# Kernel tuning notes

Hardware: AMD Instinct MI355X
Metric: run time of the kernel (lower is better)

Reference implementation:

```python
import jax, jax.numpy as jnp
import numpy as np

CONV1_T = 15.0
CONV2_T = 10.0
K2, R2 = 8, 1

def conv2d(x, w):
    # x: [T,C,H,W] (time as batch), w: [O,I,kh,kw], VALID conv (SpykeTorch Convolution = F.conv2d)
    return jax.lax.conv_general_dilated(x, w, (1, 1), 'VALID',
                                        dimension_numbers=('NCHW', 'OIHW', 'NCHW'))

def pad2(x, p):
    return jnp.pad(x, ((0, 0), (0, 0), (p, p), (p, p)))

def maxpool(x, k, s):
    return jax.lax.reduce_window(x, -jnp.inf, jax.lax.max,
                                 (1, 1, k, k), (1, 1, s, s), 'VALID')

def fire(pot, thr):
    # torch.threshold_(pot, thr, 0): keep value iff value > thr
    tp = jnp.where(pot > thr, pot, 0.0)
    return jnp.sign(tp), tp

def pointwise_inhibition(pot):
    # pot: [T,C,H,W] thresholded potentials (>=0). At each spatial position, only the
    # channel that spikes earliest (ties broken by max potential) survives.
    T, C, H, W = pot.shape
    maxval = jnp.max(pot, axis=1, keepdims=True)                    # [T,1,H,W]
    argmax = jnp.argmax(pot, axis=1, keepdims=True)                 # [T,1,H,W]
    clamp = jnp.sign(maxval)                                        # spike indicator per t
    first_t = jnp.clip((T - clamp.sum(axis=0, keepdims=True)).astype(jnp.int32), 0, T - 1)  # [1,1,H,W]
    winners = jnp.take_along_axis(argmax, first_t, axis=0)          # [1,1,H,W] winning channel
    spiked = clamp[-1:]                                             # [1,1,H,W] any spike at all
    ch = jnp.arange(C).reshape(1, C, 1, 1)
    coef = jnp.where(ch == winners, spiked, 0.0)                    # [1,C,H,W] one-hot * spiked
    return pot * coef

def get_k_winners(pot, spikes, kwta, radius):
    # Iterative k-winner selection with per-winner feature suppression and
    # columnar (spatial) inhibition of radius `radius`. Returns [kwta,3] (c,h,w), -1 if invalid.
    T, C, H, W = pot.shape
    first_t = jnp.clip((T - spikes.sum(axis=0, keepdims=True)).astype(jnp.int32), 0, T - 1)
    values = jnp.take_along_axis(pot, first_t, axis=0)              # earliest potential per (c,h,w)
    trunc = spikes * values
    v = jnp.max(trunc) * T
    trunc = trunc + spikes * v                                      # earlier spikes -> larger sum
    total = trunc.sum(axis=0)                                       # [C,H,W]

    rows = jnp.arange(H)[None, :, None]
    cols = jnp.arange(W)[None, None, :]
    chs = jnp.arange(C)[:, None, None]

    def step(total, _):
        flat = total.reshape(-1)
        idx = jnp.argmax(flat)
        max_val = flat[idx]
        c = idx // (H * W)
        h = (idx % (H * W)) // W
        w = idx % W
        valid = max_val != 0
        mask = (chs == c)
        if radius > 0:
            mask = mask | ((jnp.abs(rows - h) <= radius) & (jnp.abs(cols - w) <= radius))
        new_total = jnp.where(valid & mask, 0.0, total)
        winner = jnp.where(valid,
                           jnp.stack([c, h, w]).astype(jnp.int32),
                           jnp.full((3,), -1, jnp.int32))
        return new_total, winner

    _, winners = jax.lax.scan(step, total, None, length=kwta)
    return winners  # [kwta,3]

def setup_inputs() -> dict:
    key = jax.random.key(0)
    ka, kb, kc = jax.random.split(key, 3)
    T, C, H, W = 15, 6, 256, 256
    # cumulative (spike-wise accumulated) binary spike trains, SpykeTorch convention
    events = (jax.random.uniform(ka, (T, C, H, W)) < 0.02).astype(jnp.float32)
    x = jnp.sign(jnp.cumsum(events, axis=0))
    w1 = 0.8 + 0.05 * jax.random.normal(kb, (30, 6, 5, 5), dtype=jnp.float32)
    w2 = 0.8 + 0.05 * jax.random.normal(kc, (250, 30, 3, 3), dtype=jnp.float32)
    return {"x": x, "w1": w1, "w2": w2, "max_layer": 2}

def reference(x, w1, w2, max_layer):
    # training path, max_layer == 2 (static)
    x = pad2(x, 2)
    pot = conv2d(x, w1)                                  # [15,30,256,256]
    spk, pot = fire(pot, CONV1_T)
    spk_in = pad2(maxpool(spk, 2, 2), 1)                 # [15,30,130,130]
    pot = conv2d(spk_in, w2)                             # [15,250,128,128]
    spk, pot = fire(pot, CONV2_T)
    pot = pointwise_inhibition(pot)
    spk = jnp.sign(pot)
    winners = get_k_winners(pot, spk, K2, R2)
    return spk, pot, winners
```

## Files before the change

kernel.cpp:

```cpp
#include <hip/hip_runtime.h>
#include <cstdint>
#include <cstddef>

#define HW 16384
typedef float v2f __attribute__((ext_vector_type(2)));
typedef __attribute__((ext_vector_type(4))) float f32x4_t;
typedef __attribute__((ext_vector_type(8))) short bf16x8;

__device__ __forceinline__ unsigned short f2bf(float f) {
  unsigned int u = __float_as_uint(f);
  unsigned int r = (u + 0x7FFFu + ((u >> 16) & 1u)) >> 16;
  return (unsigned short)r;
}

__global__ __launch_bounds__(256) void k_packw(const float* __restrict__ w1,
                                               const float* __restrict__ w2,
                                               v2f* __restrict__ w1p,
                                               unsigned short* __restrict__ Wpk) {
  int g = blockIdx.x * 256 + threadIdx.x;
  if (g < 9216) {
    int mt = g / 576;
    int rem = g - mt * 576;
    int kc = rem >> 6, lane = rem & 63;
    int oc = mt * 16 + (lane & 15);
    unsigned int hbits[4], mbits[4], lbits[4];
#pragma unroll
    for (int p = 0; p < 4; ++p) { hbits[p] = 0; mbits[p] = 0; lbits[p] = 0; }
#pragma unroll
    for (int jj = 0; jj < 8; ++jj) {
      int k = kc * 32 + ((lane >> 4) << 3) + jj;
      float val = (oc < 250 && k < 270) ? w2[(size_t)oc * 270 + k] : 0.f;
      unsigned short h = f2bf(val);
      float r1 = val - __uint_as_float((unsigned int)h << 16);
      unsigned short m = f2bf(r1);
      float r2 = r1 - __uint_as_float((unsigned int)m << 16);
      unsigned short l = f2bf(r2);
      hbits[jj >> 1] |= (unsigned int)h << ((jj & 1) * 16);
      mbits[jj >> 1] |= (unsigned int)m << ((jj & 1) * 16);
      lbits[jj >> 1] |= (unsigned int)l << ((jj & 1) * 16);
    }
    size_t off = (size_t)g * 24;
    *(uint4*)&Wpk[off] = make_uint4(hbits[0], hbits[1], hbits[2], hbits[3]);
    *(uint4*)&Wpk[off + 8] = make_uint4(mbits[0], mbits[1], mbits[2], mbits[3]);
    *(uint4*)&Wpk[off + 16] = make_uint4(lbits[0], lbits[1], lbits[2], lbits[3]);
    return;
  }
  int i = g - 9216;
  if (i < 2250) {
    int m = i % 3, k = (i / 3) % 25, ic = (i / 75) % 6, ocg = i / 450;
    int g0 = ocg * 6 + 2 * m;
    w1p[i] = (v2f){w1[(g0 * 6 + ic) * 25 + k], w1[((g0 + 1) * 6 + ic) * 25 + k]};
  }
}

__global__ __launch_bounds__(256, 4) void k_conv1(const float* __restrict__ x,
                                                  const v2f* __restrict__ w1p,
                                                  uint8_t* __restrict__ spk_pool) {
  const int tile = blockIdx.x, ocg = blockIdx.y, t = blockIdx.z;
  const int oc0 = ocg * 6;
  const int tid = threadIdx.x;
  const int tx = tid & 15, ty = tid >> 4;
  const int px0 = (tile & 7) << 4, py0 = (tile >> 3) << 4;
  __shared__ float sx[2][36 * 38];
  const int iy0 = (py0 << 1) - 2, ix0 = (px0 << 1) - 2;

  int goff[6], soff[6];
  bool act[6];
#pragma unroll
  for (int j = 0; j < 6; ++j) {
    int idx = tid + 256 * j;
    bool a = idx < 1296;
    int r = idx / 36, c = idx - r * 36;
    int gy = iy0 + r, gx = ix0 + c;
    bool inb = a && (unsigned)gy < 256u && (unsigned)gx < 256u;
    goff[j] = inb ? ((gy << 8) + gx) : -1;
    soff[j] = a ? (r * 38 + c) : 0;
    act[j] = a;
  }

  v2f acc2[3][4];
#pragma unroll
  for (int m = 0; m < 3; ++m)
#pragma unroll
    for (int j = 0; j < 4; ++j) acc2[m][j] = (v2f){0.f, 0.f};

  const float* xt = x + ((size_t)(t * 6) << 16);
  float v[6];
#pragma unroll
  for (int j = 0; j < 6; ++j) v[j] = (goff[j] >= 0) ? xt[goff[j]] : 0.f;
#pragma unroll
  for (int j = 0; j < 6; ++j)
    if (act[j]) sx[0][soff[j]] = v[j];
  __syncthreads();

  for (int ic = 0; ic < 6; ++ic) {
    const int cur = ic & 1, nxt = cur ^ 1;
    if (ic < 5) {
      const float* xp = xt + ((size_t)(ic + 1) << 16);
#pragma unroll
      for (int j = 0; j < 6; ++j) v[j] = (goff[j] >= 0) ? xp[goff[j]] : 0.f;
    }
    float win_[6][6];
#pragma unroll
    for (int r = 0; r < 6; ++r) {
      float2 a = *(const float2*)&sx[cur][(2 * ty + r) * 38 + 2 * tx];
      float2 b = *(const float2*)&sx[cur][(2 * ty + r) * 38 + 2 * tx + 2];
      float2 c = *(const float2*)&sx[cur][(2 * ty + r) * 38 + 2 * tx + 4];
      win_[r][0] = a.x; win_[r][1] = a.y; win_[r][2] = b.x;
      win_[r][3] = b.y; win_[r][4] = c.x; win_[r][5] = c.y;
    }
    const v2f* wp = w1p + ((size_t)(ocg * 6 + ic) * 25) * 3;
#pragma unroll
    for (int k = 0; k < 25; ++k) {
      const int ky = k / 5, kx = k % 5;
      v2f s0 = (v2f){win_[ky][kx], win_[ky][kx]};
      v2f s1 = (v2f){win_[ky][kx + 1], win_[ky][kx + 1]};
      v2f s2 = (v2f){win_[ky + 1][kx], win_[ky + 1][kx]};
      v2f s3 = (v2f){win_[ky + 1][kx + 1], win_[ky + 1][kx + 1]};
#pragma unroll
      for (int m = 0; m < 3; ++m) {
        v2f wv = wp[k * 3 + m];
        acc2[m][0] += wv * s0;
        acc2[m][1] += wv * s1;
        acc2[m][2] += wv * s2;
        acc2[m][3] += wv * s3;
      }
    }
    if (ic < 5) {
#pragma unroll
      for (int j = 0; j < 6; ++j)
        if (act[j]) sx[nxt][soff[j]] = v[j];
    }
    __syncthreads();
  }
#pragma unroll
  for (int g = 0; g < 6; ++g) {
    const int m = g >> 1;
    float a0 = (g & 1) ? acc2[m][0].y : acc2[m][0].x;
    float a1 = (g & 1) ? acc2[m][1].y : acc2[m][1].x;
    float a2 = (g & 1) ? acc2[m][2].y : acc2[m][2].x;
    float a3 = (g & 1) ? acc2[m][3].y : acc2[m][3].x;
    int spike = (a0 > 15.f) || (a1 > 15.f) || (a2 > 15.f) || (a3 > 15.f);
    spk_pool[((size_t)(t * 30 + oc0 + g) << 14) + ((size_t)(py0 + ty) << 7) + (px0 + tx)] =
        (uint8_t)spike;
  }
}

__global__ __launch_bounds__(256, 3) void k_conv2(const uint8_t* __restrict__ spk_pool,
                                                  const unsigned short* __restrict__ Wpk,
                                                  float* __restrict__ pot2,
                                                  unsigned long long* __restrict__ mp) {
  const int nt = blockIdx.x, t = blockIdx.y;
  const int y = nt >> 1, x0 = (nt & 1) << 6;
  const int tid = threadIdx.x;
  __shared__ unsigned short Bs[64 * 288];
  __shared__ unsigned char raw[30 * 3 * 68];
  __shared__ unsigned long long mx[64];
  if (tid < 64) mx[tid] = 0ULL;

  for (int idx = tid; idx < 30 * 204; idx += 256) {
    int ic = idx / 204;
    int rem = idx - ic * 204;
    int row = rem / 68, col = rem - row * 68;
    int gy = y - 1 + row, gx = x0 - 1 + col;
    unsigned char v = 0;
    if ((unsigned)gy < 128u && (unsigned)gx < 128u && col < 67)
      v = spk_pool[((size_t)(t * 30 + ic) << 14) + (gy << 7) + gx];
    raw[idx] = v;
  }
  __syncthreads();

  {
    const int n = tid & 63, q = tid >> 6;
#pragma unroll
    for (int c = 0; c < 9; ++c) {
      unsigned int bits[4] = {0u, 0u, 0u, 0u};
#pragma unroll
      for (int e = 0; e < 8; ++e) {
        const int m = c * 8 + e;
        const int mc = m / 9, tap = m - mc * 9;
        const int dy = tap / 3, dx = tap - dy * 3;
        const int ic = q * 8 + mc;
        unsigned int v = 0u;
        if (ic < 30)
          v = raw[ic * 204 + dy * 68 + n + dx] ? 0x3F80u : 0u;
        bits[e >> 1] |= v << ((e & 1) * 16);
      }
      *(uint4*)&Bs[n * 288 + q * 72 + c * 8] = make_uint4(bits[0], bits[1], bits[2], bits[3]);
    }
  }
  __syncthreads();

  const int w = tid >> 6, lane = tid & 63;
  const int bcol = lane & 15, bq = lane >> 4;
  f32x4_t acc[4][4];
#pragma unroll
  for (int i = 0; i < 4; ++i)
#pragma unroll
    for (int j = 0; j < 4; ++j) acc[i][j] = (f32x4_t){0.f, 0.f, 0.f, 0.f};

  for (int kc = 0; kc < 9; ++kc) {
    bf16x8 bb[4];
#pragma unroll
    for (int j = 0; j < 4; ++j)
      bb[j] = *(const bf16x8*)&Bs[(j * 16 + bcol) * 288 + kc * 32 + bq * 8];
    bf16x8 ah[4], am[4], al[4];
#pragma unroll
    for (int i = 0; i < 4; ++i) {
      const size_t off = (size_t)(((w * 4 + i) * 9 + kc) * 64 + lane) * 24;
      ah[i] = *(const bf16x8*)&Wpk[off];
      am[i] = *(const bf16x8*)&Wpk[off + 8];
      al[i] = *(const bf16x8*)&Wpk[off + 16];
    }
#pragma unroll
    for (int i = 0; i < 4; ++i)
#pragma unroll
      for (int j = 0; j < 4; ++j) {
        acc[i][j] = __builtin_amdgcn_mfma_f32_16x16x32_bf16(ah[i], bb[j], acc[i][j], 0, 0, 0);
        acc[i][j] = __builtin_amdgcn_mfma_f32_16x16x32_bf16(am[i], bb[j], acc[i][j], 0, 0, 0);
        acc[i][j] = __builtin_amdgcn_mfma_f32_16x16x32_bf16(al[i], bb[j], acc[i][j], 0, 0, 0);
      }
  }

#pragma unroll
  for (int j = 0; j < 4; ++j) {
    const int loc = (y << 7) + x0 + j * 16 + bcol;
    unsigned long long best = 0ULL;
#pragma unroll
    for (int i = 0; i < 4; ++i) {
      const int mt = w * 4 + i;
#pragma unroll
      for (int r = 0; r < 4; ++r) {
        const int oc = mt * 16 + (bq << 2) + r;
        float v = acc[i][j][r];
        v = v > 10.f ? v : 0.f;
        if (oc < 250) {
          pot2[((size_t)(t * 250 + oc) << 14) + loc] = v;
          unsigned long long pk =
              ((unsigned long long)__float_as_uint(v) << 32) |
              (unsigned long long)(1023 - oc);
          best = pk > best ? pk : best;
        }
      }
    }
    atomicMax(&mx[j * 16 + bcol], best);
  }
  __syncthreads();
  if (tid < 64) mp[(size_t)t * HW + (y << 7) + x0 + tid] = mx[tid];
}

__global__ __launch_bounds__(64) void k_inhib(const float* __restrict__ pot2,
                                              const unsigned long long* __restrict__ mp,
                                              int* __restrict__ win,
                                              float* __restrict__ nspv,
                                              float* __restrict__ valv,
                                              float* __restrict__ sv) {
  const int loc = (blockIdx.x << 6) + threadIdx.x;
  int cnt = 0;
  float last = 0.f;
  unsigned long long pks[15];
#pragma unroll
  for (int t = 0; t < 15; ++t) {
    pks[t] = mp[t * HW + loc];
    float v = __uint_as_float((unsigned)(pks[t] >> 32));
    cnt += (v > 0.f) ? 1 : 0;
    if (t == 14) last = v;
  }
  const int spiked = (last > 0.f) ? 1 : 0;
  int ft = 15 - cnt;
  if (ft > 14) ft = 14;
  if (ft < 0) ft = 0;
  int wc = 1023 - (int)(pks[ft] & 1023ULL);
  if ((unsigned)wc > 249u) wc = 0;
  int nsp = 0;
#pragma unroll
  for (int t = 0; t < 15; ++t) {
    float v = pot2[((size_t)(t * 250 + wc) << 14) + loc];
    v = spiked ? v : 0.f;
    sv[t * HW + loc] = v;
    nsp += (v > 0.f) ? 1 : 0;
  }
  int ft2 = 15 - nsp;
  if (ft2 > 14) ft2 = 14;
  float value = spiked ? pot2[((size_t)(ft2 * 250 + wc) << 14) + loc] : 0.f;
  win[loc] = spiked ? wc : -1;
  nspv[loc] = (float)nsp;
  valv[loc] = value;
}

__global__ __launch_bounds__(256) void k_final(const int* __restrict__ win,
                                               const float* __restrict__ sv,
                                               float* __restrict__ spk_out,
                                               float* __restrict__ pot_out) {
  const int t = blockIdx.y;
  const int loc = (blockIdx.x << 8) + threadIdx.x;
  const int wcL = win[loc];
  const float v = sv[t * HW + loc];
  const float s = (v > 0.f) ? 1.f : 0.f;
  float* pp = pot_out + ((size_t)(t * 250) << 14) + loc;
  float* sp = spk_out + ((size_t)(t * 250) << 14) + loc;
  for (int c = 0; c < 250; ++c) {
    pp[(size_t)c << 14] = (c == wcL) ? v : 0.f;
    sp[(size_t)c << 14] = (c == wcL) ? s : 0.f;
  }
}

__global__ __launch_bounds__(256) void k_select(const int* __restrict__ win,
                                                const float* __restrict__ nspv,
                                                const float* __restrict__ valv,
                                                float* __restrict__ winners) {
  __shared__ float tot[HW];
  __shared__ int wchan[HW];
  __shared__ float redV[256];
  __shared__ int redK[256];
  __shared__ float bcValid[1];
  __shared__ int bcKey[1];
  const int tid = threadIdx.x;

  float lmax = 0.f;
  for (int i = tid; i < HW; i += 256) {
    wchan[i] = win[i];
    lmax = fmaxf(lmax, valv[i]);
  }
  redV[tid] = lmax;
  __syncthreads();
  for (int s = 128; s > 0; s >>= 1) {
    if (tid < s) redV[tid] = fmaxf(redV[tid], redV[tid + s]);
    __syncthreads();
  }
  const float v15 = redV[0] * 15.f;
  __syncthreads();
  for (int i = tid; i < HW; i += 256) tot[i] = nspv[i] * (valv[i] + v15);
  __syncthreads();

  for (int k = 0; k < 8; ++k) {
    float bv = -1.f;
    int bkey = 0x7fffffff;
    for (int i = tid; i < HW; i += 256) {
      float v = tot[i];
      int key = (wchan[i] << 14) + i;
      if (v > bv || (v == bv && key < bkey)) { bv = v; bkey = key; }
    }
    redV[tid] = bv;
    redK[tid] = bkey;
    __syncthreads();
    for (int s = 128; s > 0; s >>= 1) {
      if (tid < s) {
        float ov = redV[tid + s];
        int ok = redK[tid + s];
        if (ov > redV[tid] || (ov == redV[tid] && ok < redK[tid])) {
          redV[tid] = ov;
          redK[tid] = ok;
        }
      }
      __syncthreads();
    }
    if (tid == 0) {
      float mv = redV[0];
      int mk = redK[0];
      int valid = (mv != 0.f) ? 1 : 0;
      int c = mk >> 14, l = mk & (HW - 1);
      winners[k * 3 + 0] = valid ? (float)c : -1.f;
      winners[k * 3 + 1] = valid ? (float)(l >> 7) : -1.f;
      winners[k * 3 + 2] = valid ? (float)(l & 127) : -1.f;
      bcValid[0] = valid ? 1.f : 0.f;
      bcKey[0] = mk;
    }
    __syncthreads();
    if (bcValid[0] > 0.f) {
      int mk = bcKey[0];
      int c = mk >> 14, h = (mk & (HW - 1)) >> 7, w = mk & 127;
      for (int i = tid; i < HW; i += 256) {
        int hh = i >> 7, ww = i & 127;
        int dh = hh - h; if (dh < 0) dh = -dh;
        int dw = ww - w; if (dw < 0) dw = -dw;
        bool m = (wchan[i] == c) || (dh <= 1 && dw <= 1);
        if (m) tot[i] = 0.f;
      }
    }
    __syncthreads();
  }
}

extern "C" void kernel_launch(void* const* d_in, const int* in_sizes, int n_in,
                              void* d_out, int out_size, void* d_ws, size_t ws_size,
                              hipStream_t stream) {
  const float* x = (const float*)d_in[0];
  const float* w1 = (const float*)d_in[1];
  const float* w2 = (const float*)d_in[2];
  (void)in_sizes; (void)n_in; (void)out_size; (void)ws_size;

  float* spk_out = (float*)d_out;
  float* pot_out = spk_out + 61440000;
  float* winners = spk_out + 122880000;

  uint8_t* ws = (uint8_t*)d_ws;
  unsigned long long* mp = (unsigned long long*)ws;
  uint8_t* spk_pool = ws + 1966080;
  int* win = (int*)(ws + 9338880);
  float* nspv = (float*)(ws + 9404416);
  float* valv = (float*)(ws + 9469952);
  float* sv = (float*)(ws + 9535488);
  unsigned short* Wpk = (unsigned short*)(ws + 9535488);
  v2f* w1p = (v2f*)(ws + 10518528);

  hipLaunchKernelGGL(k_packw, dim3(45), dim3(256), 0, stream, w1, w2, w1p, Wpk);
  hipLaunchKernelGGL(k_conv1, dim3(64, 5, 15), dim3(256), 0, stream, x, w1p, spk_pool);
  hipLaunchKernelGGL(k_conv2, dim3(256, 15), dim3(256), 0, stream, spk_pool, Wpk, pot_out, mp);
  hipLaunchKernelGGL(k_inhib, dim3(256), dim3(64), 0, stream, pot_out, mp, win, nspv, valv, sv);
  hipLaunchKernelGGL(k_final, dim3(64, 15), dim3(256), 0, stream, win, sv, spk_out, pot_out);
  hipLaunchKernelGGL(k_select, dim3(1), dim3(256), 0, stream, win, nspv, valv, winners);
}
```

Baseline: 910.1 us.

## Skip empty conv2 tiles, widen conv1 channel groups, vectorize final scatter stores

conv2 now checks whether a tile's input spike window is all zero. If so, it skips building the B tile and the whole MFMA loop, writing zero potentials directly. conv1 computes 10 output channels per block instead of 6, cutting redundant input staging at the cost of more accumulator registers. k_final writes four locations per thread with float4 stores to reduce the number of store instructions on the large output fill.

```diff
diff --git a/kernel.cpp b/kernel.cpp
--- a/kernel.cpp
+++ b/kernel.cpp
@@ -47,8 +47,8 @@
   }
   int i = g - 9216;
   if (i < 2250) {
-    int m = i % 3, k = (i / 3) % 25, ic = (i / 75) % 6, ocg = i / 450;
-    int g0 = ocg * 6 + 2 * m;
+    int m = i % 5, k = (i / 5) % 25, ic = (i / 125) % 6, ocg = i / 750;
+    int g0 = ocg * 10 + 2 * m;
     w1p[i] = (v2f){w1[(g0 * 6 + ic) * 25 + k], w1[((g0 + 1) * 6 + ic) * 25 + k]};
   }
 }
@@ -57,7 +57,7 @@
                                                   const v2f* __restrict__ w1p,
                                                   uint8_t* __restrict__ spk_pool) {
   const int tile = blockIdx.x, ocg = blockIdx.y, t = blockIdx.z;
-  const int oc0 = ocg * 6;
+  const int oc0 = ocg * 10;
   const int tid = threadIdx.x;
   const int tx = tid & 15, ty = tid >> 4;
   const int px0 = (tile & 7) << 4, py0 = (tile >> 3) << 4;
@@ -78,9 +78,9 @@
     act[j] = a;
   }
 
-  v2f acc2[3][4];
-#pragma unroll
-  for (int m = 0; m < 3; ++m)
+  v2f acc2[5][4];
+#pragma unroll
+  for (int m = 0; m < 5; ++m)
 #pragma unroll
     for (int j = 0; j < 4; ++j) acc2[m][j] = (v2f){0.f, 0.f};
 
@@ -109,7 +109,7 @@
       win_[r][0] = a.x; win_[r][1] = a.y; win_[r][2] = b.x;
       win_[r][3] = b.y; win_[r][4] = c.x; win_[r][5] = c.y;
     }
-    const v2f* wp = w1p + ((size_t)(ocg * 6 + ic) * 25) * 3;
+    const v2f* wp = w1p + ((size_t)(ocg * 6 + ic) * 25) * 5;
 #pragma unroll
     for (int k = 0; k < 25; ++k) {
       const int ky = k / 5, kx = k % 5;
@@ -118,8 +118,8 @@
       v2f s2 = (v2f){win_[ky + 1][kx], win_[ky + 1][kx]};
       v2f s3 = (v2f){win_[ky + 1][kx + 1], win_[ky + 1][kx + 1]};
 #pragma unroll
-      for (int m = 0; m < 3; ++m) {
-        v2f wv = wp[k * 3 + m];
+      for (int m = 0; m < 5; ++m) {
+        v2f wv = wp[k * 5 + m];
         acc2[m][0] += wv * s0;
         acc2[m][1] += wv * s1;
         acc2[m][2] += wv * s2;
@@ -134,7 +134,7 @@
     __syncthreads();
   }
 #pragma unroll
-  for (int g = 0; g < 6; ++g) {
+  for (int g = 0; g < 10; ++g) {
     const int m = g >> 1;
     float a0 = (g & 1) ? acc2[m][0].y : acc2[m][0].x;
     float a1 = (g & 1) ? acc2[m][1].y : acc2[m][1].x;
@@ -156,8 +156,10 @@
   __shared__ unsigned short Bs[64 * 288];
   __shared__ unsigned char raw[30 * 3 * 68];
   __shared__ unsigned long long mx[64];
+  __shared__ int sFlag[4];
   if (tid < 64) mx[tid] = 0ULL;
 
+  unsigned int nz = 0;
   for (int idx = tid; idx < 30 * 204; idx += 256) {
     int ic = idx / 204;
     int rem = idx - ic * 204;
@@ -167,10 +169,24 @@
     if ((unsigned)gy < 128u && (unsigned)gx < 128u && col < 67)
       v = spk_pool[((size_t)(t * 30 + ic) << 14) + (gy << 7) + gx];
     raw[idx] = v;
-  }
-  __syncthreads();
-
+    nz |= v;
+  }
   {
+    bool wnz = __any(nz != 0);
+    if ((tid & 63) == 0) sFlag[tid >> 6] = wnz ? 1 : 0;
+  }
+  __syncthreads();
+  const int flag = sFlag[0] | sFlag[1] | sFlag[2] | sFlag[3];
+
+  const int w = tid >> 6, lane = tid & 63;
+  const int bcol = lane & 15, bq = lane >> 4;
+  f32x4_t acc[4][4];
+#pragma unroll
+  for (int i = 0; i < 4; ++i)
+#pragma unroll
+    for (int j = 0; j < 4; ++j) acc[i][j] = (f32x4_t){0.f, 0.f, 0.f, 0.f};
+
+  if (flag) {
     const int n = tid & 63, q = tid >> 6;
 #pragma unroll
     for (int c = 0; c < 9; ++c) {
@@ -188,38 +204,32 @@
       }
       *(uint4*)&Bs[n * 288 + q * 72 + c * 8] = make_uint4(bits[0], bits[1], bits[2], bits[3]);
     }
-  }
-  __syncthreads();
-
-  const int w = tid >> 6, lane = tid & 63;
-  const int bcol = lane & 15, bq = lane >> 4;
-  f32x4_t acc[4][4];
-#pragma unroll
-  for (int i = 0; i < 4; ++i)
-#pragma unroll
-    for (int j = 0; j < 4; ++j) acc[i][j] = (f32x4_t){0.f, 0.f, 0.f, 0.f};
-
-  for (int kc = 0; kc < 9; ++kc) {
-    bf16x8 bb[4];
-#pragma unroll
-    for (int j = 0; j < 4; ++j)
-      bb[j] = *(const bf16x8*)&Bs[(j * 16 + bcol) * 288 + kc * 32 + bq * 8];
-    bf16x8 ah[4], am[4], al[4];
-#pragma unroll
-    for (int i = 0; i < 4; ++i) {
-      const size_t off = (size_t)(((w * 4 + i) * 9 + kc) * 64 + lane) * 24;
-      ah[i] = *(const bf16x8*)&Wpk[off];
-      am[i] = *(const bf16x8*)&Wpk[off + 8];
-      al[i] = *(const bf16x8*)&Wpk[off + 16];
-    }
-#pragma unroll
-    for (int i = 0; i < 4; ++i)
-#pragma unroll
-      for (int j = 0; j < 4; ++j) {
-        acc[i][j] = __builtin_amdgcn_mfma_f32_16x16x32_bf16(ah[i], bb[j], acc[i][j], 0, 0, 0);
-        acc[i][j] = __builtin_amdgcn_mfma_f32_16x16x32_bf16(am[i], bb[j], acc[i][j], 0, 0, 0);
-        acc[i][j] = __builtin_amdgcn_mfma_f32_16x16x32_bf16(al[i], bb[j], acc[i][j], 0, 0, 0);
-      }
+    __syncthreads();
+
+#pragma unroll 3
+    for (int kc = 0; kc < 9; ++kc) {
+      bf16x8 bb[4];
+#pragma unroll
+      for (int j = 0; j < 4; ++j)
+        bb[j] = *(const bf16x8*)&Bs[(j * 16 + bcol) * 288 + kc * 32 + bq * 8];
+      bf16x8 ah[4], am[4], al[4];
+#pragma unroll
+      for (int i = 0; i < 4; ++i) {
+        const size_t off = (size_t)(((w * 4 + i) * 9 + kc) * 64 + lane) * 24;
+        ah[i] = *(const bf16x8*)&Wpk[off];
+        am[i] = *(const bf16x8*)&Wpk[off + 8];
+        al[i] = *(const bf16x8*)&Wpk[off + 16];
+      }
+#pragma unroll
+      for (int i = 0; i < 4; ++i)
+#pragma unroll
+        for (int j = 0; j < 4; ++j) {
+          acc[i][j] = __builtin_amdgcn_mfma_f32_16x16x32_bf16(ah[i], bb[j], acc[i][j], 0, 0, 0);
+          acc[i][j] = __builtin_amdgcn_mfma_f32_16x16x32_bf16(am[i], bb[j], acc[i][j], 0, 0, 0);
+          acc[i][j] = __builtin_amdgcn_mfma_f32_16x16x32_bf16(al[i], bb[j], acc[i][j], 0, 0, 0);
+        }
+    }
+    __syncthreads();
   }
 
 #pragma unroll
@@ -293,15 +303,24 @@
                                                float* __restrict__ spk_out,
                                                float* __restrict__ pot_out) {
   const int t = blockIdx.y;
-  const int loc = (blockIdx.x << 8) + threadIdx.x;
-  const int wcL = win[loc];
-  const float v = sv[t * HW + loc];
-  const float s = (v > 0.f) ? 1.f : 0.f;
-  float* pp = pot_out + ((size_t)(t * 250) << 14) + loc;
-  float* sp = spk_out + ((size_t)(t * 250) << 14) + loc;
+  const int l0 = (blockIdx.x << 10) + (threadIdx.x << 2);
+  int4 w4 = *(const int4*)&win[l0];
+  float4 v4 = *(const float4*)&sv[t * HW + l0];
+  float4 s4;
+  s4.x = (v4.x > 0.f) ? 1.f : 0.f;
+  s4.y = (v4.y > 0.f) ? 1.f : 0.f;
+  s4.z = (v4.z > 0.f) ? 1.f : 0.f;
+  s4.w = (v4.w > 0.f) ? 1.f : 0.f;
+  float* pp = pot_out + ((size_t)(t * 250) << 14) + l0;
+  float* sp = spk_out + ((size_t)(t * 250) << 14) + l0;
   for (int c = 0; c < 250; ++c) {
-    pp[(size_t)c << 14] = (c == wcL) ? v : 0.f;
-    sp[(size_t)c << 14] = (c == wcL) ? s : 0.f;
+    float4 pv, sw;
+    pv.x = (w4.x == c) ? v4.x : 0.f; sw.x = (w4.x == c) ? s4.x : 0.f;
+    pv.y = (w4.y == c) ? v4.y : 0.f; sw.y = (w4.y == c) ? s4.y : 0.f;
+    pv.z = (w4.z == c) ? v4.z : 0.f; sw.z = (w4.z == c) ? s4.z : 0.f;
+    pv.w = (w4.w == c) ? v4.w : 0.f; sw.w = (w4.w == c) ? s4.w : 0.f;
+    *(float4*)&pp[(size_t)c << 14] = pv;
+    *(float4*)&sp[(size_t)c << 14] = sw;
   }
 }
 
@@ -405,9 +424,9 @@
   v2f* w1p = (v2f*)(ws + 10518528);
 
   hipLaunchKernelGGL(k_packw, dim3(45), dim3(256), 0, stream, w1, w2, w1p, Wpk);
-  hipLaunchKernelGGL(k_conv1, dim3(64, 5, 15), dim3(256), 0, stream, x, w1p, spk_pool);
+  hipLaunchKernelGGL(k_conv1, dim3(64, 3, 15), dim3(256), 0, stream, x, w1p, spk_pool);
   hipLaunchKernelGGL(k_conv2, dim3(256, 15), dim3(256), 0, stream, spk_pool, Wpk, pot_out, mp);
   hipLaunchKernelGGL(k_inhib, dim3(256), dim3(64), 0, stream, pot_out, mp, win, nspv, valv, sv);
-  hipLaunchKernelGGL(k_final, dim3(64, 15), dim3(256), 0, stream, win, sv, spk_out, pot_out);
+  hipLaunchKernelGGL(k_final, dim3(16, 15), dim3(256), 0, stream, win, sv, spk_out, pot_out);
   hipLaunchKernelGGL(k_select, dim3(1), dim3(256), 0, stream, win, nspv, valv, winners);
 }
```

Measured after the change: 1.004 ms. 1.1x slower.
